# Kernel tuning notes

Hardware: AMD Instinct MI355X
Metric: run time of the kernel (lower is better)

## Reference

```python
import jax, jax.numpy as jnp
import numpy as np

NEG_INF = -1e9  # additive mask value for masked softmax


def setup_inputs() -> dict:
    key = jax.random.key(0)
    k1, k2, k3, k4, k5 = jax.random.split(key, 5)
    bz, rv_num, rv_len, in_feat, out_feat = 32, 10, 128, 300, 128
    seq_a = jax.random.normal(k1, (bz, rv_num, rv_len, in_feat), dtype=jnp.float32)
    seq_b = jax.random.normal(k2, (bz, rv_num, rv_len, in_feat), dtype=jnp.float32)
    mask_a = jax.random.randint(k3, (bz, rv_num, rv_len), 0, 2, dtype=jnp.int32)
    mask_b = jax.random.randint(k4, (bz, rv_num, rv_len), 0, 2, dtype=jnp.int32)
    # guarantee at least one valid position per review (avoid fully-masked rows)
    mask_a = mask_a.at[:, :, 0].set(1)
    mask_b = mask_b.at[:, :, 0].set(1)
    # FC transform params (xavier-normal-ish weight, zero bias)
    W = jax.random.normal(k5, (in_feat, out_feat), dtype=jnp.float32) * (2.0 / np.sqrt(in_feat + out_feat))
    b = jnp.zeros((out_feat,), dtype=jnp.float32)
    return {"seq_a": seq_a, "seq_b": seq_b, "mask_a": mask_a, "mask_b": mask_b, "W": W, "b": b}


def _masked_softmax(scores, mask):
    # scores: [N, L], mask: [N, L] in {0,1}
    logits = jnp.where(mask > 0, scores, NEG_INF)
    return jax.nn.softmax(logits, axis=-1)


def reference(seq_a, seq_b, mask_a, mask_b, W, b):
    bz, rv_num, rv_len, _ = seq_a.shape
    hdim = W.shape[1]
    N = bz * rv_num          # flattened batch of reviews
    M = rv_num * rv_len      # all tokens on the other side

    # FC + ReLU feature transform
    ta = jax.nn.relu(jnp.einsum('bnld,dh->bnlh', seq_a, W) + b)
    tb = jax.nn.relu(jnp.einsum('bnld,dh->bnlh', seq_b, W) + b)

    sa = ta.reshape(N, rv_len, hdim)
    sb = tb.reshape(N, rv_len, hdim)
    # expand: each review attends over ALL tokens of the other sequence in its sample
    ea = jnp.broadcast_to(ta.reshape(bz, 1, M, hdim), (bz, rv_num, M, hdim)).reshape(N, M, hdim)
    eb = jnp.broadcast_to(tb.reshape(bz, 1, M, hdim), (bz, rv_num, M, hdim)).reshape(N, M, hdim)

    # DOT interaction (no scale): affinity [N, rv_len, M]
    atob_aff = jnp.einsum('nld,nmd->nlm', sa, eb)
    btoa_aff = jnp.einsum('nld,nmd->nlm', sb, ea)

    # MEAN pooling over the other-sequence axis
    atob_scores = atob_aff.mean(axis=-1)  # [N, rv_len]
    btoa_scores = btoa_aff.mean(axis=-1)

    ma = mask_a.reshape(N, rv_len)
    mb = mask_b.reshape(N, rv_len)
    atob_w = _masked_softmax(atob_scores, ma)
    btoa_w = _masked_softmax(btoa_scores, mb)

    a_out = jnp.einsum('nl,nld->nd', atob_w, sa)
    b_out = jnp.einsum('nl,nld->nd', btoa_w, sb)
    return (a_out, b_out, atob_w, btoa_w)
```

## Files before the change

### kernel.cpp

```cpp
#include <hip/hip_runtime.h>
#include <hip/hip_bf16.h>


#define K_FEAT 300
#define H 128
#define NTOK 40960
#define NREV 320
#define TOK_PER_SAMPLE 1280
#define TM 128
#define BLKS_PER_SAMPLE 10
#define LDA 40
#define NCHUNK 10
#define WFRAG_ELEMS (NCHUNK * 4 * 4 * 64 * 8)

typedef __attribute__((ext_vector_type(8))) short bf16x8;
typedef __attribute__((ext_vector_type(4))) float f32x4;
typedef unsigned short u16;
typedef unsigned int u32;

static __device__ __forceinline__ u16 f2bf(float x) {
    u32 u = __float_as_uint(x);
    return (u16)((u + 0x7fffu + ((u >> 16) & 1u)) >> 16);
}
static __device__ __forceinline__ float bf2f(u16 s) {
    return __uint_as_float(((u32)s) << 16);
}

__global__ void wsplit_kernel(const float* __restrict__ W, u16* __restrict__ Wfrag)
{
    int i = blockIdx.x * 256 + threadIdx.x;
    if (i >= WFRAG_ELEMS) return;
    int j    = i & 7;
    int lane = (i >> 3) & 63;
    int frag = (i >> 9) & 3;
    int wave = (i >> 11) & 3;
    int c    = i >> 13;
    int nn = lane & 15, quad = lane >> 4;
    int t2 = frag >> 1, part = frag & 1;
    int h = (2 * wave + t2) * 16 + nn;
    int k = c * 32 + quad * 8 + j;
    float w = (k < K_FEAT) ? W[(size_t)k * H + h] : 0.f;
    u16 hi = f2bf(w);
    Wfrag[i] = part ? f2bf(w - bf2f(hi)) : hi;
}

__global__ __launch_bounds__(256, 3) void fc_mfma_kernel(
    const float* __restrict__ seq_a, const float* __restrict__ seq_b,
    const u16* __restrict__ Wfrag, const float* __restrict__ bias,
    u16* __restrict__ ta, u16* __restrict__ tb,
    float* __restrict__ psum_a, float* __restrict__ psum_b)
{
    __shared__ u16 Ah_s[TM * LDA];
    __shared__ u16 Al_s[TM * LDA];
    __shared__ float bias_s[H];

    int blk = blockIdx.x;
    const float* seq; u16* outp; float* psum;
    if (blk < 320) { seq = seq_a; outp = ta; psum = psum_a; }
    else           { seq = seq_b; outp = tb; psum = psum_b; blk -= 320; }

    const int tid = threadIdx.x;
    const int tok0 = blk * TM;
    const int wave = tid >> 6;
    const int lane = tid & 63;
    const int nn = lane & 15;
    const int quad = lane >> 4;

    if (tid < H) bias_s[tid] = bias[tid];

    const int st_t = tid >> 3;
    const int st_j = tid & 7;

    f32x4 acc[8][2];
#pragma unroll
    for (int m = 0; m < 8; ++m) {
        acc[m][0] = (f32x4){0.f, 0.f, 0.f, 0.f};
        acc[m][1] = (f32x4){0.f, 0.f, 0.f, 0.f};
    }

    float4 pf[4];
#pragma unroll
    for (int it = 0; it < 4; ++it) {
        int t = st_t + it * 32;
        int kk = 4 * st_j;
        pf[it] = make_float4(0.f, 0.f, 0.f, 0.f);
        if (kk + 4 <= K_FEAT)
            pf[it] = *(const float4*)&seq[(size_t)(tok0 + t) * K_FEAT + kk];
    }
#pragma unroll
    for (int it = 0; it < 4; ++it) {
        int t = st_t + it * 32;
        float4 v = pf[it];
        u16 h0 = f2bf(v.x), h1 = f2bf(v.y), h2 = f2bf(v.z), h3 = f2bf(v.w);
        uint2 hp, lp;
        hp.x = (u32)h0 | ((u32)h1 << 16);
        hp.y = (u32)h2 | ((u32)h3 << 16);
        lp.x = (u32)f2bf(v.x - bf2f(h0)) | ((u32)f2bf(v.y - bf2f(h1)) << 16);
        lp.y = (u32)f2bf(v.z - bf2f(h2)) | ((u32)f2bf(v.w - bf2f(h3)) << 16);
        *(uint2*)&Ah_s[t * LDA + 4 * st_j] = hp;
        *(uint2*)&Al_s[t * LDA + 4 * st_j] = lp;
    }
    __syncthreads();

    for (int c = 0; c < NCHUNK; ++c) {
        if (c < NCHUNK - 1) {
#pragma unroll
            for (int it = 0; it < 4; ++it) {
                int t = st_t + it * 32;
                int kk = (c + 1) * 32 + 4 * st_j;
                pf[it] = make_float4(0.f, 0.f, 0.f, 0.f);
                if (kk + 4 <= K_FEAT)
                    pf[it] = *(const float4*)&seq[(size_t)(tok0 + t) * K_FEAT + kk];
            }
        }
        const u16* wf = Wfrag + (size_t)(c * 4 + wave) * 2048;
        bf16x8 bh0 = *(const bf16x8*)&wf[0 * 512 + lane * 8];
        bf16x8 bl0 = *(const bf16x8*)&wf[1 * 512 + lane * 8];
        bf16x8 bh1 = *(const bf16x8*)&wf[2 * 512 + lane * 8];
        bf16x8 bl1 = *(const bf16x8*)&wf[3 * 512 + lane * 8];
#pragma unroll
        for (int m = 0; m < 8; ++m) {
            bf16x8 a_hi = *(const bf16x8*)&Ah_s[(m * 16 + nn) * LDA + quad * 8];
            bf16x8 a_lo = *(const bf16x8*)&Al_s[(m * 16 + nn) * LDA + quad * 8];
            acc[m][0] = __builtin_amdgcn_mfma_f32_16x16x32_bf16(bh0, a_hi, acc[m][0], 0, 0, 0);
            acc[m][0] = __builtin_amdgcn_mfma_f32_16x16x32_bf16(bl0, a_hi, acc[m][0], 0, 0, 0);
            acc[m][0] = __builtin_amdgcn_mfma_f32_16x16x32_bf16(bh0, a_lo, acc[m][0], 0, 0, 0);
            acc[m][1] = __builtin_amdgcn_mfma_f32_16x16x32_bf16(bh1, a_hi, acc[m][1], 0, 0, 0);
            acc[m][1] = __builtin_amdgcn_mfma_f32_16x16x32_bf16(bl1, a_hi, acc[m][1], 0, 0, 0);
            acc[m][1] = __builtin_amdgcn_mfma_f32_16x16x32_bf16(bh1, a_lo, acc[m][1], 0, 0, 0);
        }
        __syncthreads();
        if (c < NCHUNK - 1) {
#pragma unroll
            for (int it = 0; it < 4; ++it) {
                int t = st_t + it * 32;
                float4 v = pf[it];
                u16 h0 = f2bf(v.x), h1 = f2bf(v.y), h2 = f2bf(v.z), h3 = f2bf(v.w);
                uint2 hp, lp;
                hp.x = (u32)h0 | ((u32)h1 << 16);
                hp.y = (u32)h2 | ((u32)h3 << 16);
                lp.x = (u32)f2bf(v.x - bf2f(h0)) | ((u32)f2bf(v.y - bf2f(h1)) << 16);
                lp.y = (u32)f2bf(v.z - bf2f(h2)) | ((u32)f2bf(v.w - bf2f(h3)) << 16);
                *(uint2*)&Ah_s[t * LDA + 4 * st_j] = hp;
                *(uint2*)&Al_s[t * LDA + 4 * st_j] = lp;
            }
            __syncthreads();
        }
    }

#pragma unroll
    for (int ht = 0; ht < 2; ++ht) {
        int h0 = (2 * wave + ht) * 16 + quad * 4;
        float4 bb = *(const float4*)&bias_s[h0];
        float fs[4] = {0.f, 0.f, 0.f, 0.f};
#pragma unroll
        for (int tt = 0; tt < 8; ++tt) {
            int tok = tok0 + tt * 16 + nn;
            float v0 = fmaxf(acc[tt][ht][0] + bb.x, 0.f);
            float v1 = fmaxf(acc[tt][ht][1] + bb.y, 0.f);
            float v2 = fmaxf(acc[tt][ht][2] + bb.z, 0.f);
            float v3 = fmaxf(acc[tt][ht][3] + bb.w, 0.f);
            fs[0] += v0; fs[1] += v1; fs[2] += v2; fs[3] += v3;
            uint2 p;
            p.x = (u32)f2bf(v0) | ((u32)f2bf(v1) << 16);
            p.y = (u32)f2bf(v2) | ((u32)f2bf(v3) << 16);
            *(uint2*)&outp[(size_t)tok * H + h0] = p;
        }
#pragma unroll
        for (int r = 0; r < 4; ++r) {
            fs[r] += __shfl_xor(fs[r], 1);
            fs[r] += __shfl_xor(fs[r], 2);
            fs[r] += __shfl_xor(fs[r], 4);
            fs[r] += __shfl_xor(fs[r], 8);
        }
        if (nn == 0) {
#pragma unroll
            for (int r = 0; r < 4; ++r)
                psum[(size_t)blk * H + h0 + r] = fs[r];
        }
    }
}

__global__ __launch_bounds__(256) void attn_kernel(
    const u16* __restrict__ ta, const u16* __restrict__ tb,
    const int* __restrict__ mask_a, const int* __restrict__ mask_b,
    const float* __restrict__ psum_a, const float* __restrict__ psum_b,
    float* __restrict__ out)
{
    int n = blockIdx.x;
    int side = 0;
    if (n >= NREV) { side = 1; n -= NREV; }

    const u16* t = side ? tb : ta;
    const int* mask = side ? mask_b : mask_a;
    const float* psum_o = side ? psum_a : psum_b;
    float* out_vec = out + (side ? NREV * H : 0);
    float* out_w = out + 2 * NREV * H + (side ? NREV * H : 0);

    int sample = n / 10;
    int tid = threadIdx.x;

    __shared__ float score_part[128 * 17];
    __shared__ float mean_s[128];
    __shared__ float w_s[128];
    __shared__ float red[4];
    __shared__ float part_out[16 * 128];

    if (tid < 128) {
        float s = 0.f;
        const float* pb = psum_o + (size_t)sample * BLKS_PER_SAMPLE * H + tid;
#pragma unroll
        for (int i = 0; i < BLKS_PER_SAMPLE; ++i) s += pb[(size_t)i * H];
        mean_s[tid] = s * (1.0f / (float)TOK_PER_SAMPLE);
    }
    __syncthreads();

    const u16* rowbase = t + (size_t)n * 128 * H;

#pragma unroll
    for (int i = 0; i < 8; ++i) {
        int q = tid + 256 * i;
        int r = q >> 4;
        int c8 = q & 15;
        uint4 v = *(const uint4*)&rowbase[r * H + c8 * 8];
        const float* m = &mean_s[c8 * 8];
        float p = 0.f;
        p += bf2f((u16)(v.x & 0xffff)) * m[0];
        p += bf2f((u16)(v.x >> 16)) * m[1];
        p += bf2f((u16)(v.y & 0xffff)) * m[2];
        p += bf2f((u16)(v.y >> 16)) * m[3];
        p += bf2f((u16)(v.z & 0xffff)) * m[4];
        p += bf2f((u16)(v.z >> 16)) * m[5];
        p += bf2f((u16)(v.w & 0xffff)) * m[6];
        p += bf2f((u16)(v.w >> 16)) * m[7];
        score_part[r * 17 + c8] = p;
    }
    __syncthreads();

    float logit = -1e9f;
    if (tid < 128) {
        float s = 0.f;
#pragma unroll
        for (int j = 0; j < 16; ++j) s += score_part[tid * 17 + j];
        int mv = mask[n * 128 + tid];
        logit = (mv > 0) ? s : -1e9f;
    }

    float mx = logit;
    for (int off = 32; off > 0; off >>= 1) mx = fmaxf(mx, __shfl_xor(mx, off));
    if ((tid & 63) == 0) red[tid >> 6] = mx;
    __syncthreads();
    mx = fmaxf(fmaxf(red[0], red[1]), fmaxf(red[2], red[3]));
    __syncthreads();

    float e = __expf(logit - mx);
    float ssum = e;
    for (int off = 32; off > 0; off >>= 1) ssum += __shfl_xor(ssum, off);
    if ((tid & 63) == 0) red[tid >> 6] = ssum;
    __syncthreads();
    ssum = red[0] + red[1] + red[2] + red[3];

    float w = e / ssum;
    if (tid < 128) {
        w_s[tid] = w;
        out_w[n * 128 + tid] = w;
    }
    __syncthreads();

    int c8 = tid & 15;
    int lp = tid >> 4;
    float o[8] = {0.f, 0.f, 0.f, 0.f, 0.f, 0.f, 0.f, 0.f};
#pragma unroll
    for (int k = 0; k < 8; ++k) {
        int l = k * 16 + lp;
        float wl = w_s[l];
        uint4 v = *(const uint4*)&rowbase[l * H + c8 * 8];
        o[0] = fmaf(wl, bf2f((u16)(v.x & 0xffff)), o[0]);
        o[1] = fmaf(wl, bf2f((u16)(v.x >> 16)), o[1]);
        o[2] = fmaf(wl, bf2f((u16)(v.y & 0xffff)), o[2]);
        o[3] = fmaf(wl, bf2f((u16)(v.y >> 16)), o[3]);
        o[4] = fmaf(wl, bf2f((u16)(v.z & 0xffff)), o[4]);
        o[5] = fmaf(wl, bf2f((u16)(v.z >> 16)), o[5]);
        o[6] = fmaf(wl, bf2f((u16)(v.w & 0xffff)), o[6]);
        o[7] = fmaf(wl, bf2f((u16)(v.w >> 16)), o[7]);
    }
    *(float4*)&part_out[lp * 128 + c8 * 8] = make_float4(o[0], o[1], o[2], o[3]);
    *(float4*)&part_out[lp * 128 + c8 * 8 + 4] = make_float4(o[4], o[5], o[6], o[7]);
    __syncthreads();
    if (tid < 128) {
        float s = 0.f;
#pragma unroll
        for (int p = 0; p < 16; ++p) s += part_out[p * 128 + tid];
        out_vec[n * 128 + tid] = s;
    }
}

extern "C" void kernel_launch(void* const* d_in, const int* in_sizes, int n_in,
                              void* d_out, int out_size, void* d_ws, size_t ws_size,
                              hipStream_t stream)
{
    const float* seq_a = (const float*)d_in[0];
    const float* seq_b = (const float*)d_in[1];
    const int* mask_a = (const int*)d_in[2];
    const int* mask_b = (const int*)d_in[3];
    const float* W = (const float*)d_in[4];
    const float* bias = (const float*)d_in[5];
    float* out = (float*)d_out;

    u16* ta = (u16*)d_ws;
    u16* tb = ta + (size_t)NTOK * H;
    float* psum_a = (float*)(tb + (size_t)NTOK * H);
    float* psum_b = psum_a + NREV * H;
    u16* Wfrag = (u16*)(psum_b + NREV * H);

    wsplit_kernel<<<(WFRAG_ELEMS + 255) / 256, 256, 0, stream>>>(W, Wfrag);
    fc_mfma_kernel<<<640, 256, 0, stream>>>(seq_a, seq_b, Wfrag, bias, ta, tb, psum_a, psum_b);
    attn_kernel<<<640, 256, 0, stream>>>(ta, tb, mask_a, mask_b, psum_a, psum_b, out);
}
```

Before: 162.0 us.

## Fuse FC and attention kernels with a grid barrier, keeping activations in registers

Merges the FC/MFMA kernel and the attention kernel into one launch. Each block keeps its transformed 128x128 tile in accumulator registers and never writes the bf16 intermediate to global memory. A software grid-wide barrier (an atomic counter plus spin-wait) waits until all per-block column sums are published, and then scores, softmax and the weighted sum are computed straight from the registers. This removes the round trip of the intermediate tensors and one launch. In exchange, correctness depends on all 640 blocks being co-resident (3 per CU), and an extra barrier-init launch is added.

```diff
diff --git a/kernel.cpp b/kernel.cpp
--- a/kernel.cpp
+++ b/kernel.cpp
@@ -4,14 +4,13 @@
 
 #define K_FEAT 300
 #define H 128
-#define NTOK 40960
 #define NREV 320
 #define TOK_PER_SAMPLE 1280
 #define TM 128
-#define BLKS_PER_SAMPLE 10
 #define LDA 40
 #define NCHUNK 10
 #define WFRAG_ELEMS (NCHUNK * 4 * 4 * 64 * 8)
+#define NBLOCKS (2 * NREV)
 
 typedef __attribute__((ext_vector_type(8))) short bf16x8;
 typedef __attribute__((ext_vector_type(4))) float f32x4;
@@ -24,6 +23,11 @@
 }
 static __device__ __forceinline__ float bf2f(u16 s) {
     return __uint_as_float(((u32)s) << 16);
+}
+
+__global__ void bar_init_kernel(u32* __restrict__ bar)
+{
+    if (threadIdx.x == 0) *bar = 0u;
 }
 
 __global__ void wsplit_kernel(const float* __restrict__ W, u16* __restrict__ Wfrag)
@@ -44,23 +48,32 @@
     Wfrag[i] = part ? f2bf(w - bf2f(hi)) : hi;
 }
 
-__global__ __launch_bounds__(256, 3) void fc_mfma_kernel(
+__global__ __launch_bounds__(256, 3) void fused_kernel(
     const float* __restrict__ seq_a, const float* __restrict__ seq_b,
     const u16* __restrict__ Wfrag, const float* __restrict__ bias,
-    u16* __restrict__ ta, u16* __restrict__ tb,
-    float* __restrict__ psum_a, float* __restrict__ psum_b)
+    const int* __restrict__ mask_a, const int* __restrict__ mask_b,
+    float* __restrict__ psum_a, float* __restrict__ psum_b,
+    u32* __restrict__ bar,
+    float* __restrict__ out)
 {
     __shared__ u16 Ah_s[TM * LDA];
     __shared__ u16 Al_s[TM * LDA];
     __shared__ float bias_s[H];
-
-    int blk = blockIdx.x;
-    const float* seq; u16* outp; float* psum;
-    if (blk < 320) { seq = seq_a; outp = ta; psum = psum_a; }
-    else           { seq = seq_b; outp = tb; psum = psum_b; blk -= 320; }
+    __shared__ float mean_s[H];
+    __shared__ float score_part[128 * 4];
+    __shared__ float w_s[128];
+    __shared__ float red[4];
+
+    int n = blockIdx.x;
+    int side = (n >= NREV) ? 1 : 0;
+    int r = n - side * NREV;
+    int sample = r / 10;
+    const float* seq = side ? seq_b : seq_a;
+    const int* mask = side ? mask_b : mask_a;
+    float* psum = side ? psum_b : psum_a;
 
     const int tid = threadIdx.x;
-    const int tok0 = blk * TM;
+    const int tok0 = r * TM;
     const int wave = tid >> 6;
     const int lane = tid & 63;
     const int nn = lane & 15;
@@ -148,104 +161,86 @@
         }
     }
 
+    float4 bb0 = *(const float4*)&bias_s[(2 * wave + 0) * 16 + quad * 4];
+    float4 bb1 = *(const float4*)&bias_s[(2 * wave + 1) * 16 + quad * 4];
+#pragma unroll
+    for (int tt = 0; tt < 8; ++tt) {
+        acc[tt][0][0] = fmaxf(acc[tt][0][0] + bb0.x, 0.f);
+        acc[tt][0][1] = fmaxf(acc[tt][0][1] + bb0.y, 0.f);
+        acc[tt][0][2] = fmaxf(acc[tt][0][2] + bb0.z, 0.f);
+        acc[tt][0][3] = fmaxf(acc[tt][0][3] + bb0.w, 0.f);
+        acc[tt][1][0] = fmaxf(acc[tt][1][0] + bb1.x, 0.f);
+        acc[tt][1][1] = fmaxf(acc[tt][1][1] + bb1.y, 0.f);
+        acc[tt][1][2] = fmaxf(acc[tt][1][2] + bb1.z, 0.f);
+        acc[tt][1][3] = fmaxf(acc[tt][1][3] + bb1.w, 0.f);
+    }
+
 #pragma unroll
     for (int ht = 0; ht < 2; ++ht) {
         int h0 = (2 * wave + ht) * 16 + quad * 4;
-        float4 bb = *(const float4*)&bias_s[h0];
         float fs[4] = {0.f, 0.f, 0.f, 0.f};
 #pragma unroll
         for (int tt = 0; tt < 8; ++tt) {
-            int tok = tok0 + tt * 16 + nn;
-            float v0 = fmaxf(acc[tt][ht][0] + bb.x, 0.f);
-            float v1 = fmaxf(acc[tt][ht][1] + bb.y, 0.f);
-            float v2 = fmaxf(acc[tt][ht][2] + bb.z, 0.f);
-            float v3 = fmaxf(acc[tt][ht][3] + bb.w, 0.f);
-            fs[0] += v0; fs[1] += v1; fs[2] += v2; fs[3] += v3;
-            uint2 p;
-            p.x = (u32)f2bf(v0) | ((u32)f2bf(v1) << 16);
-            p.y = (u32)f2bf(v2) | ((u32)f2bf(v3) << 16);
-            *(uint2*)&outp[(size_t)tok * H + h0] = p;
-        }
-#pragma unroll
-        for (int r = 0; r < 4; ++r) {
-            fs[r] += __shfl_xor(fs[r], 1);
-            fs[r] += __shfl_xor(fs[r], 2);
-            fs[r] += __shfl_xor(fs[r], 4);
-            fs[r] += __shfl_xor(fs[r], 8);
+            fs[0] += acc[tt][ht][0];
+            fs[1] += acc[tt][ht][1];
+            fs[2] += acc[tt][ht][2];
+            fs[3] += acc[tt][ht][3];
+        }
+#pragma unroll
+        for (int g = 0; g < 4; ++g) {
+            fs[g] += __shfl_xor(fs[g], 1);
+            fs[g] += __shfl_xor(fs[g], 2);
+            fs[g] += __shfl_xor(fs[g], 4);
+            fs[g] += __shfl_xor(fs[g], 8);
         }
         if (nn == 0) {
 #pragma unroll
-            for (int r = 0; r < 4; ++r)
-                psum[(size_t)blk * H + h0 + r] = fs[r];
-        }
-    }
-}
-
-__global__ __launch_bounds__(256) void attn_kernel(
-    const u16* __restrict__ ta, const u16* __restrict__ tb,
-    const int* __restrict__ mask_a, const int* __restrict__ mask_b,
-    const float* __restrict__ psum_a, const float* __restrict__ psum_b,
-    float* __restrict__ out)
-{
-    int n = blockIdx.x;
-    int side = 0;
-    if (n >= NREV) { side = 1; n -= NREV; }
-
-    const u16* t = side ? tb : ta;
-    const int* mask = side ? mask_b : mask_a;
+            for (int g = 0; g < 4; ++g)
+                __hip_atomic_store(&psum[(size_t)r * H + h0 + g], fs[g],
+                                   __ATOMIC_RELAXED, __HIP_MEMORY_SCOPE_AGENT);
+        }
+    }
+
+    __syncthreads();
+    if (tid == 0) {
+        __hip_atomic_fetch_add(bar, 1u, __ATOMIC_RELEASE, __HIP_MEMORY_SCOPE_AGENT);
+        while (__hip_atomic_load(bar, __ATOMIC_ACQUIRE, __HIP_MEMORY_SCOPE_AGENT) < (u32)NBLOCKS)
+            __builtin_amdgcn_s_sleep(8);
+    }
+    __syncthreads();
+
     const float* psum_o = side ? psum_a : psum_b;
-    float* out_vec = out + (side ? NREV * H : 0);
-    float* out_w = out + 2 * NREV * H + (side ? NREV * H : 0);
-
-    int sample = n / 10;
-    int tid = threadIdx.x;
-
-    __shared__ float score_part[128 * 17];
-    __shared__ float mean_s[128];
-    __shared__ float w_s[128];
-    __shared__ float red[4];
-    __shared__ float part_out[16 * 128];
-
-    if (tid < 128) {
+    if (tid < H) {
         float s = 0.f;
-        const float* pb = psum_o + (size_t)sample * BLKS_PER_SAMPLE * H + tid;
-#pragma unroll
-        for (int i = 0; i < BLKS_PER_SAMPLE; ++i) s += pb[(size_t)i * H];
+#pragma unroll
+        for (int i = 0; i < 10; ++i)
+            s += __hip_atomic_load(&psum_o[(size_t)sample * 10 * H + (size_t)i * H + tid],
+                                   __ATOMIC_RELAXED, __HIP_MEMORY_SCOPE_AGENT);
         mean_s[tid] = s * (1.0f / (float)TOK_PER_SAMPLE);
     }
     __syncthreads();
 
-    const u16* rowbase = t + (size_t)n * 128 * H;
-
-#pragma unroll
-    for (int i = 0; i < 8; ++i) {
-        int q = tid + 256 * i;
-        int r = q >> 4;
-        int c8 = q & 15;
-        uint4 v = *(const uint4*)&rowbase[r * H + c8 * 8];
-        const float* m = &mean_s[c8 * 8];
-        float p = 0.f;
-        p += bf2f((u16)(v.x & 0xffff)) * m[0];
-        p += bf2f((u16)(v.x >> 16)) * m[1];
-        p += bf2f((u16)(v.y & 0xffff)) * m[2];
-        p += bf2f((u16)(v.y >> 16)) * m[3];
-        p += bf2f((u16)(v.z & 0xffff)) * m[4];
-        p += bf2f((u16)(v.z >> 16)) * m[5];
-        p += bf2f((u16)(v.w & 0xffff)) * m[6];
-        p += bf2f((u16)(v.w >> 16)) * m[7];
-        score_part[r * 17 + c8] = p;
+    float4 mm0 = *(const float4*)&mean_s[(2 * wave + 0) * 16 + quad * 4];
+    float4 mm1 = *(const float4*)&mean_s[(2 * wave + 1) * 16 + quad * 4];
+#pragma unroll
+    for (int tt = 0; tt < 8; ++tt) {
+        float sp = acc[tt][0][0] * mm0.x + acc[tt][0][1] * mm0.y
+                 + acc[tt][0][2] * mm0.z + acc[tt][0][3] * mm0.w
+                 + acc[tt][1][0] * mm1.x + acc[tt][1][1] * mm1.y
+                 + acc[tt][1][2] * mm1.z + acc[tt][1][3] * mm1.w;
+        sp += __shfl_xor(sp, 16);
+        sp += __shfl_xor(sp, 32);
+        if (quad == 0) score_part[(tt * 16 + nn) * 4 + wave] = sp;
     }
     __syncthreads();
 
     float logit = -1e9f;
     if (tid < 128) {
-        float s = 0.f;
-#pragma unroll
-        for (int j = 0; j < 16; ++j) s += score_part[tid * 17 + j];
-        int mv = mask[n * 128 + tid];
+        float s = score_part[tid * 4 + 0] + score_part[tid * 4 + 1]
+                + score_part[tid * 4 + 2] + score_part[tid * 4 + 3];
+        int mv = mask[r * 128 + tid];
         logit = (mv > 0) ? s : -1e9f;
     }
-
     float mx = logit;
     for (int off = 32; off > 0; off >>= 1) mx = fmaxf(mx, __shfl_xor(mx, off));
     if ((tid & 63) == 0) red[tid >> 6] = mx;
@@ -260,38 +255,39 @@
     __syncthreads();
     ssum = red[0] + red[1] + red[2] + red[3];
 
-    float w = e / ssum;
+    float* out_w = out + 2 * NREV * H + (size_t)side * NREV * H;
+    float wgt = e / ssum;
     if (tid < 128) {
-        w_s[tid] = w;
-        out_w[n * 128 + tid] = w;
-    }
-    __syncthreads();
-
-    int c8 = tid & 15;
-    int lp = tid >> 4;
-    float o[8] = {0.f, 0.f, 0.f, 0.f, 0.f, 0.f, 0.f, 0.f};
-#pragma unroll
-    for (int k = 0; k < 8; ++k) {
-        int l = k * 16 + lp;
-        float wl = w_s[l];
-        uint4 v = *(const uint4*)&rowbase[l * H + c8 * 8];
-        o[0] = fmaf(wl, bf2f((u16)(v.x & 0xffff)), o[0]);
-        o[1] = fmaf(wl, bf2f((u16)(v.x >> 16)), o[1]);
-        o[2] = fmaf(wl, bf2f((u16)(v.y & 0xffff)), o[2]);
-        o[3] = fmaf(wl, bf2f((u16)(v.y >> 16)), o[3]);
-        o[4] = fmaf(wl, bf2f((u16)(v.z & 0xffff)), o[4]);
-        o[5] = fmaf(wl, bf2f((u16)(v.z >> 16)), o[5]);
-        o[6] = fmaf(wl, bf2f((u16)(v.w & 0xffff)), o[6]);
-        o[7] = fmaf(wl, bf2f((u16)(v.w >> 16)), o[7]);
-    }
-    *(float4*)&part_out[lp * 128 + c8 * 8] = make_float4(o[0], o[1], o[2], o[3]);
-    *(float4*)&part_out[lp * 128 + c8 * 8 + 4] = make_float4(o[4], o[5], o[6], o[7]);
-    __syncthreads();
-    if (tid < 128) {
-        float s = 0.f;
-#pragma unroll
-        for (int p = 0; p < 16; ++p) s += part_out[p * 128 + tid];
-        out_vec[n * 128 + tid] = s;
+        w_s[tid] = wgt;
+        out_w[(size_t)r * 128 + tid] = wgt;
+    }
+    __syncthreads();
+
+    float* out_vec = out + (size_t)side * NREV * H;
+#pragma unroll
+    for (int ht = 0; ht < 2; ++ht) {
+        int h0 = (2 * wave + ht) * 16 + quad * 4;
+        float po[4] = {0.f, 0.f, 0.f, 0.f};
+#pragma unroll
+        for (int tt = 0; tt < 8; ++tt) {
+            float wl = w_s[tt * 16 + nn];
+            po[0] = fmaf(wl, acc[tt][ht][0], po[0]);
+            po[1] = fmaf(wl, acc[tt][ht][1], po[1]);
+            po[2] = fmaf(wl, acc[tt][ht][2], po[2]);
+            po[3] = fmaf(wl, acc[tt][ht][3], po[3]);
+        }
+#pragma unroll
+        for (int g = 0; g < 4; ++g) {
+            po[g] += __shfl_xor(po[g], 1);
+            po[g] += __shfl_xor(po[g], 2);
+            po[g] += __shfl_xor(po[g], 4);
+            po[g] += __shfl_xor(po[g], 8);
+        }
+        if (nn == 0) {
+#pragma unroll
+            for (int g = 0; g < 4; ++g)
+                out_vec[(size_t)r * H + h0 + g] = po[g];
+        }
     }
 }
 
@@ -307,13 +303,13 @@
     const float* bias = (const float*)d_in[5];
     float* out = (float*)d_out;
 
-    u16* ta = (u16*)d_ws;
-    u16* tb = ta + (size_t)NTOK * H;
-    float* psum_a = (float*)(tb + (size_t)NTOK * H);
+    float* psum_a = (float*)d_ws;
     float* psum_b = psum_a + NREV * H;
     u16* Wfrag = (u16*)(psum_b + NREV * H);
-
+    u32* bar = (u32*)(Wfrag + WFRAG_ELEMS);
+
+    bar_init_kernel<<<1, 64, 0, stream>>>(bar);
     wsplit_kernel<<<(WFRAG_ELEMS + 255) / 256, 256, 0, stream>>>(W, Wfrag);
-    fc_mfma_kernel<<<640, 256, 0, stream>>>(seq_a, seq_b, Wfrag, bias, ta, tb, psum_a, psum_b);
-    attn_kernel<<<640, 256, 0, stream>>>(ta, tb, mask_a, mask_b, psum_a, psum_b, out);
-}
+    fused_kernel<<<NBLOCKS, 256, 0, stream>>>(seq_a, seq_b, Wfrag, bias,
+                                              mask_a, mask_b, psum_a, psum_b, bar, out);
+}
```

After: 232.9 us. 1.44x slower.

## Load FC input rows directly into MFMA registers, drop LDS staging

Applied to the files above, without the earlier changes.

The FC kernel no longer stages split-bf16 input tiles in shared memory. Each wave now owns 32 tokens and loads its A-fragments straight from global memory into registers. The W fragments are laid out per output tile and streamed from global/L2 with a one-step prefetch. This removes the LDS writes, LDS reads and per-chunk barriers, but each wave now reads all W fragments instead of a quarter of them. Per-block column sums are reduced across waves through a small shared buffer.

```diff
diff --git a/kernel.cpp b/kernel.cpp
--- a/kernel.cpp
+++ b/kernel.cpp
@@ -7,11 +7,9 @@
 #define NTOK 40960
 #define NREV 320
 #define TOK_PER_SAMPLE 1280
-#define TM 128
 #define BLKS_PER_SAMPLE 10
-#define LDA 40
 #define NCHUNK 10
-#define WFRAG_ELEMS (NCHUNK * 4 * 4 * 64 * 8)
+#define WFRAG_ELEMS (NCHUNK * 8 * 2 * 64 * 8)
 
 typedef __attribute__((ext_vector_type(8))) short bf16x8;
 typedef __attribute__((ext_vector_type(4))) float f32x4;
@@ -25,6 +23,8 @@
 static __device__ __forceinline__ float bf2f(u16 s) {
     return __uint_as_float(((u32)s) << 16);
 }
+
+union bfpack { uint4 u; bf16x8 v; };
 
 __global__ void wsplit_kernel(const float* __restrict__ W, u16* __restrict__ Wfrag)
 {
@@ -32,13 +32,11 @@
     if (i >= WFRAG_ELEMS) return;
     int j    = i & 7;
     int lane = (i >> 3) & 63;
-    int frag = (i >> 9) & 3;
-    int wave = (i >> 11) & 3;
+    int part = (i >> 9) & 1;
+    int n    = (i >> 10) & 7;
     int c    = i >> 13;
-    int nn = lane & 15, quad = lane >> 4;
-    int t2 = frag >> 1, part = frag & 1;
-    int h = (2 * wave + t2) * 16 + nn;
-    int k = c * 32 + quad * 8 + j;
+    int h = n * 16 + (lane & 15);
+    int k = c * 32 + (lane >> 4) * 8 + j;
     float w = (k < K_FEAT) ? W[(size_t)k * H + h] : 0.f;
     u16 hi = f2bf(w);
     Wfrag[i] = part ? f2bf(w - bf2f(hi)) : hi;
@@ -50,8 +48,7 @@
     u16* __restrict__ ta, u16* __restrict__ tb,
     float* __restrict__ psum_a, float* __restrict__ psum_b)
 {
-    __shared__ u16 Ah_s[TM * LDA];
-    __shared__ u16 Al_s[TM * LDA];
+    __shared__ float psum_s[4][H];
     __shared__ float bias_s[H];
 
     int blk = blockIdx.x;
@@ -60,7 +57,7 @@
     else           { seq = seq_b; outp = tb; psum = psum_b; blk -= 320; }
 
     const int tid = threadIdx.x;
-    const int tok0 = blk * TM;
+    const int tok0 = blk * 128;
     const int wave = tid >> 6;
     const int lane = tid & 63;
     const int nn = lane & 15;
@@ -68,117 +65,112 @@
 
     if (tid < H) bias_s[tid] = bias[tid];
 
-    const int st_t = tid >> 3;
-    const int st_j = tid & 7;
-
-    f32x4 acc[8][2];
-#pragma unroll
-    for (int m = 0; m < 8; ++m) {
-        acc[m][0] = (f32x4){0.f, 0.f, 0.f, 0.f};
-        acc[m][1] = (f32x4){0.f, 0.f, 0.f, 0.f};
-    }
-
-    float4 pf[4];
-#pragma unroll
-    for (int it = 0; it < 4; ++it) {
-        int t = st_t + it * 32;
-        int kk = 4 * st_j;
-        pf[it] = make_float4(0.f, 0.f, 0.f, 0.f);
-        if (kk + 4 <= K_FEAT)
-            pf[it] = *(const float4*)&seq[(size_t)(tok0 + t) * K_FEAT + kk];
-    }
-#pragma unroll
-    for (int it = 0; it < 4; ++it) {
-        int t = st_t + it * 32;
-        float4 v = pf[it];
-        u16 h0 = f2bf(v.x), h1 = f2bf(v.y), h2 = f2bf(v.z), h3 = f2bf(v.w);
-        uint2 hp, lp;
-        hp.x = (u32)h0 | ((u32)h1 << 16);
-        hp.y = (u32)h2 | ((u32)h3 << 16);
-        lp.x = (u32)f2bf(v.x - bf2f(h0)) | ((u32)f2bf(v.y - bf2f(h1)) << 16);
-        lp.y = (u32)f2bf(v.z - bf2f(h2)) | ((u32)f2bf(v.w - bf2f(h3)) << 16);
-        *(uint2*)&Ah_s[t * LDA + 4 * st_j] = hp;
-        *(uint2*)&Al_s[t * LDA + 4 * st_j] = lp;
-    }
-    __syncthreads();
+    const float* row0 = seq + (size_t)(tok0 + wave * 32 + nn) * K_FEAT;
+    const float* row1 = row0 + (size_t)16 * K_FEAT;
+
+    f32x4 acc[2][8];
+#pragma unroll
+    for (int mi = 0; mi < 2; ++mi)
+#pragma unroll
+        for (int n = 0; n < 8; ++n) acc[mi][n] = (f32x4){0.f, 0.f, 0.f, 0.f};
+
+    float4 pf[2][2];
+    {
+        int kk = quad * 8;
+        pf[0][0] = *(const float4*)&row0[kk];
+        pf[0][1] = *(const float4*)&row0[kk + 4];
+        pf[1][0] = *(const float4*)&row1[kk];
+        pf[1][1] = *(const float4*)&row1[kk + 4];
+    }
 
     for (int c = 0; c < NCHUNK; ++c) {
+        bf16x8 ah[2], al[2];
+#pragma unroll
+        for (int mi = 0; mi < 2; ++mi) {
+            float v[8] = {pf[mi][0].x, pf[mi][0].y, pf[mi][0].z, pf[mi][0].w,
+                          pf[mi][1].x, pf[mi][1].y, pf[mi][1].z, pf[mi][1].w};
+            u16 hh[8];
+            bfpack ph, pl;
+#pragma unroll
+            for (int j = 0; j < 8; ++j) hh[j] = f2bf(v[j]);
+            ph.u.x = (u32)hh[0] | ((u32)hh[1] << 16);
+            ph.u.y = (u32)hh[2] | ((u32)hh[3] << 16);
+            ph.u.z = (u32)hh[4] | ((u32)hh[5] << 16);
+            ph.u.w = (u32)hh[6] | ((u32)hh[7] << 16);
+            pl.u.x = (u32)f2bf(v[0] - bf2f(hh[0])) | ((u32)f2bf(v[1] - bf2f(hh[1])) << 16);
+            pl.u.y = (u32)f2bf(v[2] - bf2f(hh[2])) | ((u32)f2bf(v[3] - bf2f(hh[3])) << 16);
+            pl.u.z = (u32)f2bf(v[4] - bf2f(hh[4])) | ((u32)f2bf(v[5] - bf2f(hh[5])) << 16);
+            pl.u.w = (u32)f2bf(v[6] - bf2f(hh[6])) | ((u32)f2bf(v[7] - bf2f(hh[7])) << 16);
+            ah[mi] = ph.v;
+            al[mi] = pl.v;
+        }
         if (c < NCHUNK - 1) {
-#pragma unroll
-            for (int it = 0; it < 4; ++it) {
-                int t = st_t + it * 32;
-                int kk = (c + 1) * 32 + 4 * st_j;
-                pf[it] = make_float4(0.f, 0.f, 0.f, 0.f);
-                if (kk + 4 <= K_FEAT)
-                    pf[it] = *(const float4*)&seq[(size_t)(tok0 + t) * K_FEAT + kk];
+            int kk = (c + 1) * 32 + quad * 8;
+            float4 z = make_float4(0.f, 0.f, 0.f, 0.f);
+            pf[0][0] = (kk + 4 <= K_FEAT) ? *(const float4*)&row0[kk] : z;
+            pf[0][1] = (kk + 8 <= K_FEAT) ? *(const float4*)&row0[kk + 4] : z;
+            pf[1][0] = (kk + 4 <= K_FEAT) ? *(const float4*)&row1[kk] : z;
+            pf[1][1] = (kk + 8 <= K_FEAT) ? *(const float4*)&row1[kk + 4] : z;
+        }
+        const u16* wbase = Wfrag + (size_t)c * (8 * 2 * 512);
+        bf16x8 wh = *(const bf16x8*)&wbase[0 * 1024 + 0 + lane * 8];
+        bf16x8 wl = *(const bf16x8*)&wbase[0 * 1024 + 512 + lane * 8];
+#pragma unroll
+        for (int n = 0; n < 8; ++n) {
+            bf16x8 whc = wh, wlc = wl;
+            if (n < 7) {
+                wh = *(const bf16x8*)&wbase[(n + 1) * 1024 + 0 + lane * 8];
+                wl = *(const bf16x8*)&wbase[(n + 1) * 1024 + 512 + lane * 8];
             }
-        }
-        const u16* wf = Wfrag + (size_t)(c * 4 + wave) * 2048;
-        bf16x8 bh0 = *(const bf16x8*)&wf[0 * 512 + lane * 8];
-        bf16x8 bl0 = *(const bf16x8*)&wf[1 * 512 + lane * 8];
-        bf16x8 bh1 = *(const bf16x8*)&wf[2 * 512 + lane * 8];
-        bf16x8 bl1 = *(const bf16x8*)&wf[3 * 512 + lane * 8];
-#pragma unroll
-        for (int m = 0; m < 8; ++m) {
-            bf16x8 a_hi = *(const bf16x8*)&Ah_s[(m * 16 + nn) * LDA + quad * 8];
-            bf16x8 a_lo = *(const bf16x8*)&Al_s[(m * 16 + nn) * LDA + quad * 8];
-            acc[m][0] = __builtin_amdgcn_mfma_f32_16x16x32_bf16(bh0, a_hi, acc[m][0], 0, 0, 0);
-            acc[m][0] = __builtin_amdgcn_mfma_f32_16x16x32_bf16(bl0, a_hi, acc[m][0], 0, 0, 0);
-            acc[m][0] = __builtin_amdgcn_mfma_f32_16x16x32_bf16(bh0, a_lo, acc[m][0], 0, 0, 0);
-            acc[m][1] = __builtin_amdgcn_mfma_f32_16x16x32_bf16(bh1, a_hi, acc[m][1], 0, 0, 0);
-            acc[m][1] = __builtin_amdgcn_mfma_f32_16x16x32_bf16(bl1, a_hi, acc[m][1], 0, 0, 0);
-            acc[m][1] = __builtin_amdgcn_mfma_f32_16x16x32_bf16(bh1, a_lo, acc[m][1], 0, 0, 0);
-        }
-        __syncthreads();
-        if (c < NCHUNK - 1) {
-#pragma unroll
-            for (int it = 0; it < 4; ++it) {
-                int t = st_t + it * 32;
-                float4 v = pf[it];
-                u16 h0 = f2bf(v.x), h1 = f2bf(v.y), h2 = f2bf(v.z), h3 = f2bf(v.w);
-                uint2 hp, lp;
-                hp.x = (u32)h0 | ((u32)h1 << 16);
-                hp.y = (u32)h2 | ((u32)h3 << 16);
-                lp.x = (u32)f2bf(v.x - bf2f(h0)) | ((u32)f2bf(v.y - bf2f(h1)) << 16);
-                lp.y = (u32)f2bf(v.z - bf2f(h2)) | ((u32)f2bf(v.w - bf2f(h3)) << 16);
-                *(uint2*)&Ah_s[t * LDA + 4 * st_j] = hp;
-                *(uint2*)&Al_s[t * LDA + 4 * st_j] = lp;
-            }
-            __syncthreads();
-        }
-    }
-
-#pragma unroll
-    for (int ht = 0; ht < 2; ++ht) {
-        int h0 = (2 * wave + ht) * 16 + quad * 4;
-        float4 bb = *(const float4*)&bias_s[h0];
-        float fs[4] = {0.f, 0.f, 0.f, 0.f};
-#pragma unroll
-        for (int tt = 0; tt < 8; ++tt) {
-            int tok = tok0 + tt * 16 + nn;
-            float v0 = fmaxf(acc[tt][ht][0] + bb.x, 0.f);
-            float v1 = fmaxf(acc[tt][ht][1] + bb.y, 0.f);
-            float v2 = fmaxf(acc[tt][ht][2] + bb.z, 0.f);
-            float v3 = fmaxf(acc[tt][ht][3] + bb.w, 0.f);
-            fs[0] += v0; fs[1] += v1; fs[2] += v2; fs[3] += v3;
+            acc[0][n] = __builtin_amdgcn_mfma_f32_16x16x32_bf16(whc, ah[0], acc[0][n], 0, 0, 0);
+            acc[0][n] = __builtin_amdgcn_mfma_f32_16x16x32_bf16(wlc, ah[0], acc[0][n], 0, 0, 0);
+            acc[0][n] = __builtin_amdgcn_mfma_f32_16x16x32_bf16(whc, al[0], acc[0][n], 0, 0, 0);
+            acc[1][n] = __builtin_amdgcn_mfma_f32_16x16x32_bf16(whc, ah[1], acc[1][n], 0, 0, 0);
+            acc[1][n] = __builtin_amdgcn_mfma_f32_16x16x32_bf16(wlc, ah[1], acc[1][n], 0, 0, 0);
+            acc[1][n] = __builtin_amdgcn_mfma_f32_16x16x32_bf16(whc, al[1], acc[1][n], 0, 0, 0);
+        }
+    }
+
+#pragma unroll
+    for (int n = 0; n < 8; ++n) {
+        float4 bb = *(const float4*)&bias_s[n * 16 + quad * 4];
+#pragma unroll
+        for (int mi = 0; mi < 2; ++mi) {
+            int tok = tok0 + (wave * 2 + mi) * 16 + nn;
+            float v0 = fmaxf(acc[mi][n][0] + bb.x, 0.f);
+            float v1 = fmaxf(acc[mi][n][1] + bb.y, 0.f);
+            float v2 = fmaxf(acc[mi][n][2] + bb.z, 0.f);
+            float v3 = fmaxf(acc[mi][n][3] + bb.w, 0.f);
+            acc[mi][n][0] = v0; acc[mi][n][1] = v1;
+            acc[mi][n][2] = v2; acc[mi][n][3] = v3;
             uint2 p;
             p.x = (u32)f2bf(v0) | ((u32)f2bf(v1) << 16);
             p.y = (u32)f2bf(v2) | ((u32)f2bf(v3) << 16);
-            *(uint2*)&outp[(size_t)tok * H + h0] = p;
-        }
-#pragma unroll
-        for (int r = 0; r < 4; ++r) {
-            fs[r] += __shfl_xor(fs[r], 1);
-            fs[r] += __shfl_xor(fs[r], 2);
-            fs[r] += __shfl_xor(fs[r], 4);
-            fs[r] += __shfl_xor(fs[r], 8);
-        }
+            *(uint2*)&outp[(size_t)tok * H + n * 16 + quad * 4] = p;
+        }
+    }
+
+#pragma unroll
+    for (int n = 0; n < 8; ++n) {
+        float s0 = acc[0][n][0] + acc[1][n][0];
+        float s1 = acc[0][n][1] + acc[1][n][1];
+        float s2 = acc[0][n][2] + acc[1][n][2];
+        float s3 = acc[0][n][3] + acc[1][n][3];
+        s0 += __shfl_xor(s0, 1); s0 += __shfl_xor(s0, 2); s0 += __shfl_xor(s0, 4); s0 += __shfl_xor(s0, 8);
+        s1 += __shfl_xor(s1, 1); s1 += __shfl_xor(s1, 2); s1 += __shfl_xor(s1, 4); s1 += __shfl_xor(s1, 8);
+        s2 += __shfl_xor(s2, 1); s2 += __shfl_xor(s2, 2); s2 += __shfl_xor(s2, 4); s2 += __shfl_xor(s2, 8);
+        s3 += __shfl_xor(s3, 1); s3 += __shfl_xor(s3, 2); s3 += __shfl_xor(s3, 4); s3 += __shfl_xor(s3, 8);
         if (nn == 0) {
-#pragma unroll
-            for (int r = 0; r < 4; ++r)
-                psum[(size_t)blk * H + h0 + r] = fs[r];
-        }
-    }
+            psum_s[wave][n * 16 + quad * 4 + 0] = s0;
+            psum_s[wave][n * 16 + quad * 4 + 1] = s1;
+            psum_s[wave][n * 16 + quad * 4 + 2] = s2;
+            psum_s[wave][n * 16 + quad * 4 + 3] = s3;
+        }
+    }
+    __syncthreads();
+    if (tid < H)
+        psum[(size_t)blk * H + tid] = psum_s[0][tid] + psum_s[1][tid]
+                                    + psum_s[2][tid] + psum_s[3][tid];
 }
 
 __global__ __launch_bounds__(256) void attn_kernel(
```

Result: slower. 173.8 us (+7.3%).
